# Optimization experiments

Measured on AMD Instinct MI355X. Metric: run time of the kernel, lower is better.

The kernel has to match this reference:

```python
import jax, jax.numpy as jnp
import numpy as np

N, D, C, E, K = 100000, 64, 40, 1600000, 2

def setup_inputs() -> dict:
    key = jax.random.key(0)
    k1, k2, k3 = jax.random.split(key, 3)
    x = jax.random.normal(k1, (N, D), dtype=jnp.float32)
    edge_index = jax.random.randint(k2, (2, E), 0, N, dtype=jnp.int64)
    W = jax.random.normal(k3, (D, C), dtype=jnp.float32) * 0.05
    b = jnp.zeros((C,), dtype=jnp.float32)
    return {"x": x, "edge_index": edge_index, "W": W, "b": b}

def reference(x, edge_index, W, b):
    n = x.shape[0]
    self_loop = jnp.arange(n, dtype=edge_index.dtype)
    row = jnp.concatenate([edge_index[0], self_loop])  # [E+N]
    col = jnp.concatenate([edge_index[1], self_loop])  # [E+N]
    # degree over row (out-degree incl. self loops), as in torch_geometric.utils.degree
    deg = jax.ops.segment_sum(jnp.ones_like(row, dtype=x.dtype), row, num_segments=n)
    deg_inv_sqrt = jnp.where(deg > 0, jax.lax.rsqrt(deg), 0.0)
    norm = deg_inv_sqrt[row] * deg_inv_sqrt[col]  # [E+N]
    # K hops of SpMM: out[r] += norm_e * x[c] for each edge e=(r,c)
    for _ in range(K):
        x = jax.ops.segment_sum(norm[:, None] * x[col], row, num_segments=n)
    logits = x @ W + b  # [N, C]
    return jax.nn.log_softmax(logits, axis=1)
```

## Files before the change

kernel.cpp:

```cpp
#include <hip/hip_runtime.h>
#include <math.h>


#define D_FEAT 64
#define NCLS 40
#define NDW 20
#define NV4 5
#define BROWS 512
#define BROWS_LOG 9
#define BINCAP 10240
#define CSRCAP 12288
#define EPT 25

typedef float v2f __attribute__((ext_vector_type(2)));

__device__ __forceinline__ unsigned pack_bf16_2(float lo, float hi) {
    unsigned ulo = __float_as_uint(lo);
    unsigned uhi = __float_as_uint(hi);
    ulo = (ulo + 0x7fffu + ((ulo >> 16) & 1u)) >> 16;
    uhi = (uhi + 0x7fffu + ((uhi >> 16) & 1u)) & 0xffff0000u;
    return uhi | ulo;
}

__device__ __forceinline__ void acc2p(unsigned u, v2f& a) {
    v2f v;
    v.x = __uint_as_float(u << 16);
    v.y = __uint_as_float(u & 0xffff0000u);
    a += v;
}

__global__ void init_kernel(int* __restrict__ bucket_cursor,
                            unsigned* __restrict__ y0, unsigned* __restrict__ y1,
                            int n, int nb) {
    int i = threadIdx.x;
    if (i < nb) bucket_cursor[i] = 0;
    if (i < NDW) {
        y0[(size_t)n * NDW + i] = 0u;
        y1[(size_t)n * NDW + i] = 0u;
    }
}

__global__ __launch_bounds__(256) void bin_edges_kernel(const int* __restrict__ rows,
                                                        const int* __restrict__ cols,
                                                        int* __restrict__ bucket_cursor,
                                                        unsigned* __restrict__ bins,
                                                        int e, int nb) {
    __shared__ int cnt[512];
    for (int i = threadIdx.x; i < nb; i += 256) cnt[i] = 0;
    __syncthreads();
    int base = blockIdx.x * (256 * EPT) + threadIdx.x;
    int rr[EPT], cc[EPT];
#pragma unroll
    for (int k = 0; k < EPT; k++) {
        int idx = base + k * 256;
        if (idx < e) { rr[k] = rows[idx]; cc[k] = cols[idx]; }
        else { rr[k] = -1; cc[k] = 0; }
    }
#pragma unroll
    for (int k = 0; k < EPT; k++)
        if (rr[k] >= 0) atomicAdd(&cnt[rr[k] >> BROWS_LOG], 1);
    __syncthreads();
    for (int i = threadIdx.x; i < nb; i += 256) {
        int c = cnt[i];
        cnt[i] = (c > 0) ? atomicAdd(&bucket_cursor[i], c) : 0;
    }
    __syncthreads();
#pragma unroll
    for (int k = 0; k < EPT; k++) {
        if (rr[k] >= 0) {
            int b = rr[k] >> BROWS_LOG;
            int pos = atomicAdd(&cnt[b], 1);
            bins[(size_t)b * BINCAP + pos] =
                ((unsigned)(rr[k] & (BROWS - 1)) << 17) | (unsigned)cc[k];
        }
    }
}

__global__ __launch_bounds__(512) void build_csr_kernel(const unsigned* __restrict__ bins,
                                                        const int* __restrict__ bucket_cursor,
                                                        int* __restrict__ csr_col,
                                                        uint2* __restrict__ row_info,
                                                        float* __restrict__ dis,
                                                        uint4* __restrict__ pinfo, int n) {
    __shared__ int cnt[512];
    __shared__ int sm[512];
    __shared__ int cur[512];
    __shared__ int lcsr[CSRCAP];
    int b = blockIdx.x;
    int tid = threadIdx.x;
    int m = bucket_cursor[b];
    cnt[tid] = 0;
    __syncthreads();
    const unsigned* bp = bins + (size_t)b * BINCAP;
    for (int i = tid; i < m; i += 512) atomicAdd(&cnt[bp[i] >> 17], 1);
    __syncthreads();
    int c = cnt[tid];
    int padded = (c + 3) & ~3;
    int r = b * BROWS + tid;
    float dv = rsqrtf(1.0f + (float)c);
    if (r < n) dis[r] = dv;
    sm[tid] = padded;
    __syncthreads();
    for (int off = 1; off < 512; off <<= 1) {
        int t = (tid >= off) ? sm[tid - off] : 0;
        __syncthreads();
        sm[tid] += t;
        __syncthreads();
    }
    int off0 = sm[tid] - padded;
    cur[tid] = off0;
    if (r < n) row_info[r] = make_uint2((unsigned)(b * CSRCAP + off0), (unsigned)padded);
    __syncthreads();
    for (int i = tid; i < m; i += 512) {
        unsigned u = bp[i];
        int pos = atomicAdd(&cur[u >> 17], 1);
        lcsr[pos] = (int)(u & 0x1FFFFu);
    }
    __syncthreads();
    if (r < n) {
        for (int j = c; j < padded; j++) lcsr[off0 + j] = n;
    }
    __syncthreads();
    int tot = sm[511];
    int4* cp4 = (int4*)(csr_col + (size_t)b * CSRCAP);
    const int4* l4 = (const int4*)lcsr;
    for (int i = tid; i < (tot >> 2); i += 512) cp4[i] = l4[i];
    {
        int g = tot + tid;
        if (g < CSRCAP) csr_col[(size_t)b * CSRCAP + g] = n;
    }

    __syncthreads();
    if (tid < 64) cnt[tid] = 0;
    __syncthreads();
    int bin = min(padded >> 2, 63);
    if (r < n) atomicAdd(&cnt[bin], 1);
    __syncthreads();
    if (tid < 64) sm[tid] = cnt[tid];
    __syncthreads();
    for (int off = 1; off < 64; off <<= 1) {
        int t = (tid >= off && tid < 64) ? sm[tid - off] : 0;
        __syncthreads();
        if (tid < 64) sm[tid] += t;
        __syncthreads();
    }
    if (tid < 64) cur[tid] = sm[tid] - cnt[tid];
    __syncthreads();
    if (r < n) {
        int rank = atomicAdd(&cur[bin], 1);
        pinfo[b * BROWS + rank] = make_uint4((unsigned)(b * CSRCAP + off0),
                                             (unsigned)padded, (unsigned)r,
                                             __float_as_uint(dv));
    } else {
        pinfo[b * BROWS + tid] = make_uint4(0u, 0u, 0xFFFFFFFFu, 0u);
    }
}

__global__ __launch_bounds__(256) void sort_rows_kernel(int* __restrict__ csr_col,
                                                        const uint2* __restrict__ row_info,
                                                        int n) {
    int wid = (int)((blockIdx.x * blockDim.x + threadIdx.x) >> 6);
    int lane = threadIdx.x & 63;
    int r0 = wid * 2, r1 = r0 + 1;
    if (r0 >= n) return;
    uint2 i0 = row_info[r0];
    uint2 i1 = (r1 < n) ? row_info[r1] : make_uint2(0u, 0u);
    int p0 = (int)i0.y, p1 = (int)i1.y;
    if (p0 <= 32 && p1 <= 32) {
        int half = lane >> 5, hl = lane & 31;
        int base = half ? (int)i1.x : (int)i0.x;
        int pad  = half ? p1 : p0;
        int key = (hl < pad) ? csr_col[base + hl] : 0x7fffffff;
#pragma unroll
        for (int k = 2; k <= 32; k <<= 1) {
#pragma unroll
            for (int j = k >> 1; j > 0; j >>= 1) {
                int other = __shfl_xor(key, j, 64);
                bool takeMin = (((hl & j) == 0) == ((hl & k) == 0));
                int mn = min(key, other), mx = max(key, other);
                key = takeMin ? mn : mx;
            }
        }
        if (hl < pad) csr_col[base + hl] = key;
    } else {
        for (int t = 0; t < 2; t++) {
            int base = t ? (int)i1.x : (int)i0.x;
            int pad  = t ? p1 : p0;
            if (pad == 0) continue;
            if (pad <= 64) {
                int key = (lane < pad) ? csr_col[base + lane] : 0x7fffffff;
#pragma unroll
                for (int k = 2; k <= 64; k <<= 1) {
#pragma unroll
                    for (int j = k >> 1; j > 0; j >>= 1) {
                        int other = __shfl_xor(key, j, 64);
                        bool takeMin = (((lane & j) == 0) == ((lane & k) == 0));
                        int mn = min(key, other), mx = max(key, other);
                        key = takeMin ? mn : mx;
                    }
                }
                if (lane < pad) csr_col[base + lane] = key;
            } else if (lane == 0) {
                for (int i2 = 1; i2 < pad; i2++) {
                    int kk = csr_col[base + i2];
                    int j2 = i2 - 1;
                    while (j2 >= 0 && csr_col[base + j2] > kk) {
                        csr_col[base + j2 + 1] = csr_col[base + j2]; j2--;
                    }
                    csr_col[base + j2 + 1] = kk;
                }
            }
        }
    }
}

__global__ __launch_bounds__(256) void xw_kernel(const float* __restrict__ x,
                                                 const float* __restrict__ W,
                                                 const float* __restrict__ dis,
                                                 unsigned* __restrict__ y0, int n) {
    int r = blockIdx.x * 256 + threadIdx.x;
    if (r >= n) return;
    float acc[NCLS];
#pragma unroll
    for (int c = 0; c < NCLS; c++) acc[c] = 0.f;
    const float4* xp = (const float4*)(x + (size_t)r * D_FEAT);
#pragma unroll 4
    for (int dg = 0; dg < 16; dg++) {
        float4 xa = xp[dg];
#pragma unroll
        for (int j = 0; j < 4; j++) {
            float a = (j == 0) ? xa.x : (j == 1) ? xa.y : (j == 2) ? xa.z : xa.w;
            int d = dg * 4 + j;
#pragma unroll
            for (int c4 = 0; c4 < 10; c4++) {
                float4 wv = *(const float4*)(W + d * NCLS + c4 * 4);
                acc[c4 * 4 + 0] += a * wv.x;
                acc[c4 * 4 + 1] += a * wv.y;
                acc[c4 * 4 + 2] += a * wv.z;
                acc[c4 * 4 + 3] += a * wv.w;
            }
        }
    }
    float s = dis[r];
    uint4* p = (uint4*)(y0 + (size_t)r * NDW);
#pragma unroll
    for (int q = 0; q < NV4; q++) {
        uint4 o;
        o.x = pack_bf16_2(s * acc[8 * q + 0], s * acc[8 * q + 1]);
        o.y = pack_bf16_2(s * acc[8 * q + 2], s * acc[8 * q + 3]);
        o.z = pack_bf16_2(s * acc[8 * q + 4], s * acc[8 * q + 5]);
        o.w = pack_bf16_2(s * acc[8 * q + 6], s * acc[8 * q + 7]);
        p[q] = o;
    }
}

#define ACCA(u) acc2p(u.x, h0A); acc2p(u.y, h1A); acc2p(u.z, h2A); acc2p(u.w, h3A);
#define ACCB(u) acc2p(u.x, h0B); acc2p(u.y, h1B); acc2p(u.z, h2B); acc2p(u.w, h3B);
#define GATHER8(cp, xs4, gl, base, len)                                     \
    uint4 cv0 = cp[(base >> 2)], cv1 = cp[(base >> 2) + 1];                 \
    uint4 u0 = xs4[cv0.x * NV4 + gl], u1 = xs4[cv0.y * NV4 + gl];           \
    uint4 u2 = xs4[cv0.z * NV4 + gl], u3 = xs4[cv0.w * NV4 + gl];           \
    uint4 u4 = xs4[cv1.x * NV4 + gl], u5 = xs4[cv1.y * NV4 + gl];           \
    uint4 u6 = xs4[cv1.z * NV4 + gl], u7 = xs4[cv1.w * NV4 + gl];           \
    __builtin_amdgcn_sched_barrier(0);                                      \
    if (base < len)     { ACCA(u0) ACCA(u1) ACCA(u2) ACCA(u3) }             \
    if (base + 4 < len) { ACCB(u4) ACCB(u5) ACCB(u6) ACCB(u7) }

__global__ __launch_bounds__(256, 5) void spmm_hop1_kernel(const uint4* __restrict__ xs_in,
                                                           uint4* __restrict__ xs_out,
                                                           const uint4* __restrict__ pinfo,
                                                           const int* __restrict__ csr_col,
                                                           int n, int nperm) {
    int wave = (blockIdx.x * blockDim.x + threadIdx.x) >> 6;
    int lane = threadIdx.x & 63;
    int e = lane / 5;
    int gl = lane - e * 5;
    int pidx = wave * 12 + e;
    bool inb = (e < 12) && (pidx < nperm);
    uint4 info = pinfo[inb ? pidx : 0];
    int s = (int)info.x;
    int len = inb ? (int)info.y : 0;
    int r = inb ? (int)info.z : -1;
    float dr = __uint_as_float(inb ? info.w : 0u);
    int maxlen = len;
#pragma unroll
    for (int o = 1; o < 64; o <<= 1) maxlen = max(maxlen, __shfl_xor(maxlen, o, 64));

    v2f h0A = {0.f,0.f}, h1A = {0.f,0.f}, h2A = {0.f,0.f}, h3A = {0.f,0.f};
    v2f h0B = {0.f,0.f}, h1B = {0.f,0.f}, h2B = {0.f,0.f}, h3B = {0.f,0.f};
    const uint4* cp = (const uint4*)(csr_col + s);
    for (int base = 0; base < maxlen; base += 8) {
        GATHER8(cp, xs_in, gl, base, len)
    }
    if (r >= 0 && r < n) {
        v2f h0 = h0A + h0B, h1 = h1A + h1B, h2 = h2A + h2B, h3 = h3A + h3B;
        uint4 us = xs_in[r * NV4 + gl];
        acc2p(us.x, h0); acc2p(us.y, h1); acc2p(us.z, h2); acc2p(us.w, h3);
        float d2 = dr * dr;
        uint4 o;
        o.x = pack_bf16_2(d2 * h0.x, d2 * h0.y);
        o.y = pack_bf16_2(d2 * h1.x, d2 * h1.y);
        o.z = pack_bf16_2(d2 * h2.x, d2 * h2.y);
        o.w = pack_bf16_2(d2 * h3.x, d2 * h3.y);
        xs_out[r * NV4 + gl] = o;
    }
}

__global__ __launch_bounds__(256, 5) void spmm_logits_kernel(const uint4* __restrict__ xs_in,
                                                             const uint4* __restrict__ pinfo,
                                                             const int* __restrict__ csr_col,
                                                             const float* __restrict__ b,
                                                             float* __restrict__ out,
                                                             int n, int nperm) {
    int wave = (blockIdx.x * blockDim.x + threadIdx.x) >> 6;
    int lane = threadIdx.x & 63;
    int e = lane / 5;
    int gl = lane - e * 5;
    int pidx = wave * 12 + e;
    bool inb = (e < 12) && (pidx < nperm);
    uint4 info = pinfo[inb ? pidx : 0];
    int s = (int)info.x;
    int len = inb ? (int)info.y : 0;
    int r = inb ? (int)info.z : -1;
    float dr = __uint_as_float(inb ? info.w : 0u);
    int maxlen = len;
#pragma unroll
    for (int o = 1; o < 64; o <<= 1) maxlen = max(maxlen, __shfl_xor(maxlen, o, 64));

    v2f h0A = {0.f,0.f}, h1A = {0.f,0.f}, h2A = {0.f,0.f}, h3A = {0.f,0.f};
    v2f h0B = {0.f,0.f}, h1B = {0.f,0.f}, h2B = {0.f,0.f}, h3B = {0.f,0.f};
    const uint4* cp = (const uint4*)(csr_col + s);
    for (int base = 0; base < maxlen; base += 8) {
        GATHER8(cp, xs_in, gl, base, len)
    }
    v2f h0 = h0A + h0B, h1 = h1A + h1B, h2 = h2A + h2B, h3 = h3A + h3B;
    uint4 us = (r >= 0 && r < n) ? xs_in[r * NV4 + gl] : make_uint4(0u, 0u, 0u, 0u);
    acc2p(us.x, h0); acc2p(us.y, h1); acc2p(us.z, h2); acc2p(us.w, h3);

    const float4* b4 = (const float4*)b;
    float4 ba = b4[gl * 2], bb = b4[gl * 2 + 1];
    float y0 = dr * h0.x + ba.x, y1 = dr * h0.y + ba.y;
    float y2 = dr * h1.x + ba.z, y3 = dr * h1.y + ba.w;
    float y4 = dr * h2.x + bb.x, y5 = dr * h2.y + bb.y;
    float y6 = dr * h3.x + bb.z, y7 = dr * h3.y + bb.w;

    int gb = ((e < 12) ? e : 11) * 5;
    float mloc = fmaxf(fmaxf(fmaxf(y0, y1), fmaxf(y2, y3)),
                       fmaxf(fmaxf(y4, y5), fmaxf(y6, y7)));
    float M = mloc;
#pragma unroll
    for (int k = 0; k < 5; k++) M = fmaxf(M, __shfl(mloc, gb + k, 64));
    float sloc = __expf(y0 - M) + __expf(y1 - M) + __expf(y2 - M) + __expf(y3 - M) +
                 __expf(y4 - M) + __expf(y5 - M) + __expf(y6 - M) + __expf(y7 - M);
    float S = 0.f;
#pragma unroll
    for (int k = 0; k < 5; k++) S += __shfl(sloc, gb + k, 64);
    float lse = M + __logf(S);

    if (r >= 0 && r < n) {
        float4* op = (float4*)(out + (size_t)r * NCLS) + gl * 2;
        op[0] = make_float4(y0 - lse, y1 - lse, y2 - lse, y3 - lse);
        op[1] = make_float4(y4 - lse, y5 - lse, y6 - lse, y7 - lse);
    }
}

extern "C" void kernel_launch(void* const* d_in, const int* in_sizes, int n_in,
                              void* d_out, int out_size, void* d_ws, size_t ws_size,
                              hipStream_t stream) {
    const float* x  = (const float*)d_in[0];
    const int*   ei = (const int*)d_in[1];
    const float* W  = (const float*)d_in[2];
    const float* b  = (const float*)d_in[3];
    float* out = (float*)d_out;

    const int n = in_sizes[0] / D_FEAT;
    const int e = in_sizes[1] / 2;
    const int nb = (n + BROWS - 1) / BROWS;

    const int* rows = ei;
    const int* cols = ei + e;

    size_t na = ((size_t)n + 256) & ~(size_t)255;
    size_t npm = (size_t)nb * BROWS;
    int*      bucket_cursor = (int*)d_ws;
    float*    dis           = (float*)(bucket_cursor + 256);
    uint2*    row_info      = (uint2*)(dis + na);
    uint4*    pinfo         = (uint4*)(row_info + na);
    unsigned* bins          = (unsigned*)(pinfo + npm);
    int*      csr_col       = (int*)(bins + (size_t)nb * BINCAP);
    unsigned* y0            = (unsigned*)(csr_col + (size_t)nb * CSRCAP);
    unsigned* y1            = y0 + (size_t)(n + 1) * NDW;

    const int BS = 256;

    init_kernel<<<1, 256, 0, stream>>>(bucket_cursor, y0, y1, n, nb);
    {
        int blocks = (e + BS * EPT - 1) / (BS * EPT);
        bin_edges_kernel<<<blocks, BS, 0, stream>>>(rows, cols, bucket_cursor, bins, e, nb);
    }
    build_csr_kernel<<<nb, 512, 0, stream>>>(bins, bucket_cursor, csr_col, row_info, dis,
                                             pinfo, n);
    {
        int nwv = (n + 1) / 2;
        int sortBlocks = (nwv * 64 + BS - 1) / BS;
        sort_rows_kernel<<<sortBlocks, BS, 0, stream>>>(csr_col, row_info, n);
    }
    {
        int blocks = (n + BS - 1) / BS;
        xw_kernel<<<blocks, BS, 0, stream>>>(x, W, dis, y0, n);
    }

    int nperm = (int)npm;
    int nwaves = (nperm + 11) / 12;
    int blocks = (nwaves + 3) / 4;
    spmm_hop1_kernel<<<blocks, BS, 0, stream>>>((const uint4*)y0, (uint4*)y1, pinfo,
                                                csr_col, n, nperm);
    spmm_logits_kernel<<<blocks, BS, 0, stream>>>((const uint4*)y1, pinfo, csr_col,
                                                  b, out, n, nperm);
}
```

Baseline: 222.5 us.

## Merge row sort and XW into one launch, single accumulator set, raise occupancy

Fuses the per-row column sort and the dense X·W projection into one kernel by splitting the grid into block ranges, which removes one launch and lets the two independent phases run concurrently. The SpMM kernels drop the dual A/B accumulator sets in favour of a single set and raise the launch-bounds occupancy hint from 5 to 8 waves, lowering register pressure to fit more waves. Edges per thread in binning drop from 25 to 8, giving more blocks. The single accumulator chain adds a serial dependency on the adds, and the higher occupancy hint could force register spills.

```diff
diff --git a/kernel.cpp b/kernel.cpp
--- a/kernel.cpp
+++ b/kernel.cpp
@@ -10,7 +10,7 @@
 #define BROWS_LOG 9
 #define BINCAP 10240
 #define CSRCAP 12288
-#define EPT 25
+#define EPT 8
 
 typedef float v2f __attribute__((ext_vector_type(2)));
 
@@ -156,10 +156,51 @@
     }
 }
 
-__global__ __launch_bounds__(256) void sort_rows_kernel(int* __restrict__ csr_col,
-                                                        const uint2* __restrict__ row_info,
-                                                        int n) {
-    int wid = (int)((blockIdx.x * blockDim.x + threadIdx.x) >> 6);
+__global__ __launch_bounds__(256) void sort_xw_kernel(int* __restrict__ csr_col,
+                                                      const uint2* __restrict__ row_info,
+                                                      const float* __restrict__ x,
+                                                      const float* __restrict__ W,
+                                                      const float* __restrict__ dis,
+                                                      unsigned* __restrict__ y0,
+                                                      int n, int sortBlocks) {
+    if ((int)blockIdx.x >= sortBlocks) {
+        int r = ((int)blockIdx.x - sortBlocks) * 256 + threadIdx.x;
+        if (r >= n) return;
+        float acc[NCLS];
+#pragma unroll
+        for (int c = 0; c < NCLS; c++) acc[c] = 0.f;
+        const float4* xp = (const float4*)(x + (size_t)r * D_FEAT);
+#pragma unroll 4
+        for (int dg = 0; dg < 16; dg++) {
+            float4 xa = xp[dg];
+#pragma unroll
+            for (int j = 0; j < 4; j++) {
+                float a = (j == 0) ? xa.x : (j == 1) ? xa.y : (j == 2) ? xa.z : xa.w;
+                int d = dg * 4 + j;
+#pragma unroll
+                for (int c4 = 0; c4 < 10; c4++) {
+                    float4 wv = *(const float4*)(W + d * NCLS + c4 * 4);
+                    acc[c4 * 4 + 0] += a * wv.x;
+                    acc[c4 * 4 + 1] += a * wv.y;
+                    acc[c4 * 4 + 2] += a * wv.z;
+                    acc[c4 * 4 + 3] += a * wv.w;
+                }
+            }
+        }
+        float s = dis[r];
+        uint4* p = (uint4*)(y0 + (size_t)r * NDW);
+#pragma unroll
+        for (int q = 0; q < NV4; q++) {
+            uint4 o;
+            o.x = pack_bf16_2(s * acc[8 * q + 0], s * acc[8 * q + 1]);
+            o.y = pack_bf16_2(s * acc[8 * q + 2], s * acc[8 * q + 3]);
+            o.z = pack_bf16_2(s * acc[8 * q + 4], s * acc[8 * q + 5]);
+            o.w = pack_bf16_2(s * acc[8 * q + 6], s * acc[8 * q + 7]);
+            p[q] = o;
+        }
+        return;
+    }
+    int wid = ((int)blockIdx.x * 256 + (int)threadIdx.x) >> 6;
     int lane = threadIdx.x & 63;
     int r0 = wid * 2, r1 = r0 + 1;
     if (r0 >= n) return;
@@ -214,48 +255,7 @@
     }
 }
 
-__global__ __launch_bounds__(256) void xw_kernel(const float* __restrict__ x,
-                                                 const float* __restrict__ W,
-                                                 const float* __restrict__ dis,
-                                                 unsigned* __restrict__ y0, int n) {
-    int r = blockIdx.x * 256 + threadIdx.x;
-    if (r >= n) return;
-    float acc[NCLS];
-#pragma unroll
-    for (int c = 0; c < NCLS; c++) acc[c] = 0.f;
-    const float4* xp = (const float4*)(x + (size_t)r * D_FEAT);
-#pragma unroll 4
-    for (int dg = 0; dg < 16; dg++) {
-        float4 xa = xp[dg];
-#pragma unroll
-        for (int j = 0; j < 4; j++) {
-            float a = (j == 0) ? xa.x : (j == 1) ? xa.y : (j == 2) ? xa.z : xa.w;
-            int d = dg * 4 + j;
-#pragma unroll
-            for (int c4 = 0; c4 < 10; c4++) {
-                float4 wv = *(const float4*)(W + d * NCLS + c4 * 4);
-                acc[c4 * 4 + 0] += a * wv.x;
-                acc[c4 * 4 + 1] += a * wv.y;
-                acc[c4 * 4 + 2] += a * wv.z;
-                acc[c4 * 4 + 3] += a * wv.w;
-            }
-        }
-    }
-    float s = dis[r];
-    uint4* p = (uint4*)(y0 + (size_t)r * NDW);
-#pragma unroll
-    for (int q = 0; q < NV4; q++) {
-        uint4 o;
-        o.x = pack_bf16_2(s * acc[8 * q + 0], s * acc[8 * q + 1]);
-        o.y = pack_bf16_2(s * acc[8 * q + 2], s * acc[8 * q + 3]);
-        o.z = pack_bf16_2(s * acc[8 * q + 4], s * acc[8 * q + 5]);
-        o.w = pack_bf16_2(s * acc[8 * q + 6], s * acc[8 * q + 7]);
-        p[q] = o;
-    }
-}
-
-#define ACCA(u) acc2p(u.x, h0A); acc2p(u.y, h1A); acc2p(u.z, h2A); acc2p(u.w, h3A);
-#define ACCB(u) acc2p(u.x, h0B); acc2p(u.y, h1B); acc2p(u.z, h2B); acc2p(u.w, h3B);
+#define ACC1(u) acc2p(u.x, h0); acc2p(u.y, h1); acc2p(u.z, h2); acc2p(u.w, h3);
 #define GATHER8(cp, xs4, gl, base, len)                                     \
     uint4 cv0 = cp[(base >> 2)], cv1 = cp[(base >> 2) + 1];                 \
     uint4 u0 = xs4[cv0.x * NV4 + gl], u1 = xs4[cv0.y * NV4 + gl];           \
@@ -263,10 +263,10 @@
     uint4 u4 = xs4[cv1.x * NV4 + gl], u5 = xs4[cv1.y * NV4 + gl];           \
     uint4 u6 = xs4[cv1.z * NV4 + gl], u7 = xs4[cv1.w * NV4 + gl];           \
     __builtin_amdgcn_sched_barrier(0);                                      \
-    if (base < len)     { ACCA(u0) ACCA(u1) ACCA(u2) ACCA(u3) }             \
-    if (base + 4 < len) { ACCB(u4) ACCB(u5) ACCB(u6) ACCB(u7) }
-
-__global__ __launch_bounds__(256, 5) void spmm_hop1_kernel(const uint4* __restrict__ xs_in,
+    if (base < len)     { ACC1(u0) ACC1(u1) ACC1(u2) ACC1(u3) }             \
+    if (base + 4 < len) { ACC1(u4) ACC1(u5) ACC1(u6) ACC1(u7) }
+
+__global__ __launch_bounds__(256, 8) void spmm_hop1_kernel(const uint4* __restrict__ xs_in,
                                                            uint4* __restrict__ xs_out,
                                                            const uint4* __restrict__ pinfo,
                                                            const int* __restrict__ csr_col,
@@ -286,14 +286,12 @@
 #pragma unroll
     for (int o = 1; o < 64; o <<= 1) maxlen = max(maxlen, __shfl_xor(maxlen, o, 64));
 
-    v2f h0A = {0.f,0.f}, h1A = {0.f,0.f}, h2A = {0.f,0.f}, h3A = {0.f,0.f};
-    v2f h0B = {0.f,0.f}, h1B = {0.f,0.f}, h2B = {0.f,0.f}, h3B = {0.f,0.f};
+    v2f h0 = {0.f,0.f}, h1 = {0.f,0.f}, h2 = {0.f,0.f}, h3 = {0.f,0.f};
     const uint4* cp = (const uint4*)(csr_col + s);
     for (int base = 0; base < maxlen; base += 8) {
         GATHER8(cp, xs_in, gl, base, len)
     }
     if (r >= 0 && r < n) {
-        v2f h0 = h0A + h0B, h1 = h1A + h1B, h2 = h2A + h2B, h3 = h3A + h3B;
         uint4 us = xs_in[r * NV4 + gl];
         acc2p(us.x, h0); acc2p(us.y, h1); acc2p(us.z, h2); acc2p(us.w, h3);
         float d2 = dr * dr;
@@ -306,7 +304,7 @@
     }
 }
 
-__global__ __launch_bounds__(256, 5) void spmm_logits_kernel(const uint4* __restrict__ xs_in,
+__global__ __launch_bounds__(256, 8) void spmm_logits_kernel(const uint4* __restrict__ xs_in,
                                                              const uint4* __restrict__ pinfo,
                                                              const int* __restrict__ csr_col,
                                                              const float* __restrict__ b,
@@ -327,13 +325,11 @@
 #pragma unroll
     for (int o = 1; o < 64; o <<= 1) maxlen = max(maxlen, __shfl_xor(maxlen, o, 64));
 
-    v2f h0A = {0.f,0.f}, h1A = {0.f,0.f}, h2A = {0.f,0.f}, h3A = {0.f,0.f};
-    v2f h0B = {0.f,0.f}, h1B = {0.f,0.f}, h2B = {0.f,0.f}, h3B = {0.f,0.f};
+    v2f h0 = {0.f,0.f}, h1 = {0.f,0.f}, h2 = {0.f,0.f}, h3 = {0.f,0.f};
     const uint4* cp = (const uint4*)(csr_col + s);
     for (int base = 0; base < maxlen; base += 8) {
         GATHER8(cp, xs_in, gl, base, len)
     }
-    v2f h0 = h0A + h0B, h1 = h1A + h1B, h2 = h2A + h2B, h3 = h3A + h3B;
     uint4 us = (r >= 0 && r < n) ? xs_in[r * NV4 + gl] : make_uint4(0u, 0u, 0u, 0u);
     acc2p(us.x, h0); acc2p(us.y, h1); acc2p(us.z, h2); acc2p(us.w, h3);
 
@@ -403,11 +399,9 @@
     {
         int nwv = (n + 1) / 2;
         int sortBlocks = (nwv * 64 + BS - 1) / BS;
-        sort_rows_kernel<<<sortBlocks, BS, 0, stream>>>(csr_col, row_info, n);
-    }
-    {
-        int blocks = (n + BS - 1) / BS;
-        xw_kernel<<<blocks, BS, 0, stream>>>(x, W, dis, y0, n);
+        int xwBlocks = (n + BS - 1) / BS;
+        sort_xw_kernel<<<sortBlocks + xwBlocks, BS, 0, stream>>>(
+            csr_col, row_info, x, W, dis, y0, n, sortBlocks);
     }
 
     int nperm = (int)npm;
```

Result: slower. 233.7 us (+5.1%).
